# Kernel tuning notes

Hardware: AMD Instinct MI355X
Metric: run time of the kernel (lower is better)

Reference implementation:

```python
import jax, jax.numpy as jnp
import numpy as np

HID = 2048      # hidden_size
NH = 32         # num_heads
G = 8           # num_kv_groups
R = NH // G     # repeat factor (heads per kv group)
HD = HID // NH  # head_dim = 64
SCALE = HD ** 0.5


def setup_inputs() -> dict:
    key = jax.random.key(0)
    ks = jax.random.split(key, 10)
    B, S = 2, 1024
    x = jax.random.normal(ks[0], (B, S, HID), dtype=jnp.float32)
    attention_mask = jnp.ones((B, S, S), dtype=jnp.float32)
    # Linear params stored as [in, out] (y = x @ W + b), same math as torch Linear.
    Wq = jax.random.normal(ks[1], (HID, HID), dtype=jnp.float32) * 0.02
    bq = jnp.zeros((HID,), dtype=jnp.float32)
    Wk = jax.random.normal(ks[2], (HID, G * HD), dtype=jnp.float32) * 0.02
    bk = jnp.zeros((G * HD,), dtype=jnp.float32)
    Wv = jax.random.normal(ks[3], (HID, G * HD), dtype=jnp.float32) * 0.02
    bv = jnp.zeros((G * HD,), dtype=jnp.float32)
    Wo = jax.random.normal(ks[4], (HID, HID), dtype=jnp.float32) * 0.02
    bo = jnp.zeros((HID,), dtype=jnp.float32)
    return {"x": x, "attention_mask": attention_mask,
            "Wq": Wq, "bq": bq, "Wk": Wk, "bk": bk,
            "Wv": Wv, "bv": bv, "Wo": Wo, "bo": bo}


def reference(x, attention_mask, Wq, bq, Wk, bk, Wv, bv, Wo, bo):
    B, S, _ = x.shape
    # Projections. Group heads as (G, R) instead of repeat_interleave:
    # repeat_interleave(key, R, dim=2) duplicates each kv group R times, which is
    # exactly sharing key[:, :, g] across the R heads of group g.
    q = (x @ Wq + bq).reshape(B, S, G, R, HD)   # [B,S,G,R,HD] (heads = G*R in order)
    k = (x @ Wk + bk).reshape(B, S, G, HD)      # [B,S,G,HD]
    v = (x @ Wv + bv).reshape(B, S, G, HD)
    # scores [B,G,R,Sq,Sk] == torch's [B, NH, Sq, Sk] with NH = G*R
    scores = jnp.einsum('bqgrd,bkgd->bgrqk', q, k) / SCALE
    scores = scores * attention_mask[:, None, None]  # multiplicative mask per head
    w = jax.nn.softmax(scores, axis=-1)
    out = jnp.einsum('bgrqk,bkgd->bqgrd', w, v).reshape(B, S, HID)
    return out @ Wo + bo + x
```

## Files before the change

### kernel.cpp

```cpp
#include <hip/hip_runtime.h>

typedef unsigned short u16;
typedef unsigned int u32;
typedef __attribute__((ext_vector_type(8))) short bf16x8;
typedef __attribute__((ext_vector_type(4))) float f32x4;

#define HID 2048
#define S_LEN 1024
#define BATCH 2
#define G_KV 8
#define R_REP 4
#define HD 64
#define NQKV 3072

__device__ __forceinline__ u16 f2bf(float f) {
    union { u32 u; float ff; } x; x.ff = f;
    u32 u = x.u;
    u += 0x7FFFu + ((u >> 16) & 1u);
    return (u16)(u >> 16);
}
__device__ __forceinline__ float bf2f(u16 v) {
    union { u32 u; float f; } x; x.u = ((u32)v) << 16; return x.f;
}

__device__ __forceinline__ void gload_lds16(const void* g, void* l) {
    __builtin_amdgcn_global_load_lds((const __attribute__((address_space(1))) void*)g,
                                     (__attribute__((address_space(3))) void*)l,
                                     16, 0, 0);
}

__global__ __launch_bounds__(256) void cvt_x(const float* __restrict__ in,
                                             u16* __restrict__ out) {
    int i = (blockIdx.x * 256 + threadIdx.x) * 8;
    float4 a = *(const float4*)(in + i);
    float4 b = *(const float4*)(in + i + 4);
    u16 t[8] = {f2bf(a.x), f2bf(a.y), f2bf(a.z), f2bf(a.w),
                f2bf(b.x), f2bf(b.y), f2bf(b.z), f2bf(b.w)};
    *(uint4*)(out + i) = *(const uint4*)t;
}

__global__ __launch_bounds__(256) void transpose_cvt(const float* __restrict__ in,
                                                     u16* __restrict__ out,
                                                     int K, int N) {
    __shared__ float tile[32][33];
    int n0 = blockIdx.x * 32, k0 = blockIdx.y * 32;
    int tx = threadIdx.x, ty = threadIdx.y;
#pragma unroll
    for (int j = 0; j < 4; ++j)
        tile[ty + j * 8][tx] = in[(size_t)(k0 + ty + j * 8) * N + n0 + tx];
    __syncthreads();
#pragma unroll
    for (int j = 0; j < 4; ++j)
        out[(size_t)(n0 + ty + j * 8) * K + k0 + tx] = f2bf(tile[tx][ty + j * 8]);
}

__global__ __launch_bounds__(256) void gemm_qkv(const u16* __restrict__ Xb,
                                                const u16* __restrict__ WT,
                                                const float* __restrict__ bq,
                                                const float* __restrict__ bk,
                                                const float* __restrict__ bv,
                                                u16* __restrict__ qb,
                                                u16* __restrict__ kb,
                                                u16* __restrict__ vb) {
    __shared__ __align__(16) u16 As[128 * 32];
    __shared__ __align__(16) u16 Bs[128 * 32];
    int tid = threadIdx.x;
    int w = tid >> 6, lane = tid & 63, quad = lane >> 4, l16 = lane & 15;
    int m0 = blockIdx.y * 128, n0 = blockIdx.x * 128;
    int wr = (w >> 1) * 64, wc = (w & 1) * 64;
    int srow = lane >> 2, scol = (lane & 3) * 8;

    f32x4 acc[4][4];
#pragma unroll
    for (int i = 0; i < 4; ++i)
#pragma unroll
        for (int j = 0; j < 4; ++j) acc[i][j] = (f32x4){0.f, 0.f, 0.f, 0.f};

    for (int k0 = 0; k0 < 2048; k0 += 32) {
#pragma unroll
        for (int c = 0; c < 2; ++c) {
            int row = c * 64 + w * 16 + srow;
            gload_lds16(&Xb[(size_t)(m0 + row) * 2048 + k0 + scol], &As[(c * 64 + w * 16) * 32]);
            gload_lds16(&WT[(size_t)(n0 + row) * 2048 + k0 + scol], &Bs[(c * 64 + w * 16) * 32]);
        }
        __syncthreads();
        bf16x8 af[4], bfr[4];
#pragma unroll
        for (int mt = 0; mt < 4; ++mt)
            af[mt] = *(const bf16x8*)&As[(wr + mt * 16 + l16) * 32 + quad * 8];
#pragma unroll
        for (int nt = 0; nt < 4; ++nt)
            bfr[nt] = *(const bf16x8*)&Bs[(wc + nt * 16 + l16) * 32 + quad * 8];
#pragma unroll
        for (int mt = 0; mt < 4; ++mt)
#pragma unroll
            for (int nt = 0; nt < 4; ++nt)
                acc[mt][nt] = __builtin_amdgcn_mfma_f32_16x16x32_bf16(af[mt], bfr[nt], acc[mt][nt], 0, 0, 0);
        __syncthreads();
    }

#pragma unroll
    for (int nt = 0; nt < 4; ++nt) {
        int n = n0 + wc + nt * 16 + l16;
        float bias;
        if (n < 2048) bias = bq[n];
        else if (n < 2560) bias = bk[n - 2048];
        else bias = bv[n - 2560];
#pragma unroll
        for (int mt = 0; mt < 4; ++mt) {
#pragma unroll
            for (int reg = 0; reg < 4; ++reg) {
                int m = m0 + wr + mt * 16 + quad * 4 + reg;
                float val = acc[mt][nt][reg] + bias;
                int b = m >> 10, s = m & 1023;
                if (n < 2048) {
                    int g = n >> 8, r = (n >> 6) & 3, d = n & 63;
                    qb[((((size_t)(b * G_KV + g) * R_REP + r) * S_LEN) + s) * HD + d] = f2bf(val * 0.125f);
                } else if (n < 2560) {
                    int n2 = n - 2048, g = n2 >> 6, d = n2 & 63;
                    kb[(((size_t)(b * G_KV + g) * S_LEN) + s) * HD + d] = f2bf(val);
                } else {
                    int n2 = n - 2560, g = n2 >> 6, d = n2 & 63;
                    vb[(((size_t)(b * G_KV + g) * HD + d) * S_LEN) + s] = f2bf(val);
                }
            }
        }
    }
}

__global__ __launch_bounds__(256) void attn_mfma(const u16* __restrict__ qbuf,
                                                 const u16* __restrict__ kbuf,
                                                 const u16* __restrict__ vtbuf,
                                                 const u16* __restrict__ mask_bf,
                                                 u16* __restrict__ aout) {
    __shared__ __align__(16) u16 Ks[64 * 72];
    __shared__ __align__(16) u16 Vs[64 * 72];
    __shared__ __align__(16) u16 Ms[64 * 72];
    __shared__ __align__(16) u16 Ps[64 * 72];

    int d = blockIdx.x;
    int xcd = d & 7, j = d >> 3;
    int pr = xcd * 2 + (j >> 6);
    int r = (j >> 4) & 3, qblk = j & 15;
    int b = pr >> 3, g = pr & 7;

    int tid = threadIdx.x;
    int w = tid >> 6, lane = tid & 63, quad = lane >> 4, l16 = lane & 15;
    int s0 = qblk * 64;

    const u16* qrow = qbuf +
        ((((size_t)(b * G_KV + g) * R_REP + r) * S_LEN) + s0 + w * 16 + l16) * HD;
    bf16x8 qf0 = *(const bf16x8*)(qrow + quad * 8);
    bf16x8 qf1 = *(const bf16x8*)(qrow + 32 + quad * 8);

    f32x4 o_acc[4];
#pragma unroll
    for (int i = 0; i < 4; ++i) o_acc[i] = (f32x4){0.f, 0.f, 0.f, 0.f};
    float l_tot[4] = {0.f, 0.f, 0.f, 0.f};

    const u16* kbase  = kbuf  + (size_t)(b * G_KV + g) * S_LEN * HD;
    const u16* vtbase = vtbuf + (size_t)(b * G_KV + g) * HD * S_LEN;
    const u16* mbase  = mask_bf + ((size_t)b * S_LEN + s0) * S_LEN;

    int srow = tid >> 2, sc = (tid & 3) * 16;
    int prow = w * 16 + quad * 4;

    uint4 kp0, kp1, vp0, vp1, mp0, mp1;
    {
        const u16* kr = kbase + (size_t)srow * HD + sc;
        kp0 = *(const uint4*)kr; kp1 = *(const uint4*)(kr + 8);
        const u16* vr = vtbase + (size_t)srow * S_LEN + sc;
        vp0 = *(const uint4*)vr; vp1 = *(const uint4*)(vr + 8);
        const u16* mr = mbase + (size_t)srow * S_LEN + sc;
        mp0 = *(const uint4*)mr; mp1 = *(const uint4*)(mr + 8);
    }

    for (int kt = 0; kt < 16; ++kt) {
        __syncthreads();
        *(uint4*)&Ks[srow * 72 + sc]     = kp0;
        *(uint4*)&Ks[srow * 72 + sc + 8] = kp1;
        *(uint4*)&Vs[srow * 72 + sc]     = vp0;
        *(uint4*)&Vs[srow * 72 + sc + 8] = vp1;
        *(uint4*)&Ms[srow * 72 + sc]     = mp0;
        *(uint4*)&Ms[srow * 72 + sc + 8] = mp1;
        __syncthreads();

        if (kt < 15) {
            int nk = (kt + 1) * 64;
            const u16* kr = kbase + (size_t)(nk + srow) * HD + sc;
            kp0 = *(const uint4*)kr; kp1 = *(const uint4*)(kr + 8);
            const u16* vr = vtbase + (size_t)srow * S_LEN + nk + sc;
            vp0 = *(const uint4*)vr; vp1 = *(const uint4*)(vr + 8);
            const u16* mr = mbase + (size_t)srow * S_LEN + nk + sc;
            mp0 = *(const uint4*)mr; mp1 = *(const uint4*)(mr + 8);
        }

        f32x4 p[4];
#pragma unroll
        for (int nt = 0; nt < 4; ++nt) {
            bf16x8 kf0 = *(const bf16x8*)&Ks[(nt * 16 + l16) * 72 + quad * 8];
            bf16x8 kf1 = *(const bf16x8*)&Ks[(nt * 16 + l16) * 72 + 32 + quad * 8];
            f32x4 z = (f32x4){0.f, 0.f, 0.f, 0.f};
            z = __builtin_amdgcn_mfma_f32_16x16x32_bf16(qf0, kf0, z, 0, 0, 0);
            p[nt] = __builtin_amdgcn_mfma_f32_16x16x32_bf16(qf1, kf1, z, 0, 0, 0);
        }

        float part[4] = {0.f, 0.f, 0.f, 0.f};
#pragma unroll
        for (int nt = 0; nt < 4; ++nt) {
#pragma unroll
            for (int reg = 0; reg < 4; ++reg) {
                int qr = prow + reg;
                float m = bf2f(Ms[qr * 72 + nt * 16 + l16]);
                float e = __expf(p[nt][reg] * m);
                part[reg] += e;
                Ps[qr * 72 + nt * 16 + l16] = f2bf(e);
            }
        }
        __syncthreads();

#pragma unroll
        for (int reg = 0; reg < 4; ++reg) {
            float v = part[reg];
            v += __shfl_xor(v, 1);
            v += __shfl_xor(v, 2);
            v += __shfl_xor(v, 4);
            v += __shfl_xor(v, 8);
            l_tot[reg] += v;
        }

        bf16x8 pf0 = *(const bf16x8*)&Ps[(w * 16 + l16) * 72 + quad * 8];
        bf16x8 pf1 = *(const bf16x8*)&Ps[(w * 16 + l16) * 72 + 32 + quad * 8];
#pragma unroll
        for (int nt = 0; nt < 4; ++nt) {
            bf16x8 vf0 = *(const bf16x8*)&Vs[(nt * 16 + l16) * 72 + quad * 8];
            bf16x8 vf1 = *(const bf16x8*)&Vs[(nt * 16 + l16) * 72 + 32 + quad * 8];
            o_acc[nt] = __builtin_amdgcn_mfma_f32_16x16x32_bf16(pf0, vf0, o_acc[nt], 0, 0, 0);
            o_acc[nt] = __builtin_amdgcn_mfma_f32_16x16x32_bf16(pf1, vf1, o_acc[nt], 0, 0, 0);
        }
    }

#pragma unroll
    for (int reg = 0; reg < 4; ++reg) {
        int row = prow + reg;
        float inv = 1.0f / l_tot[reg];
        int sidx = s0 + row;
        u16* dst = aout + ((size_t)(b * S_LEN + sidx)) * HID + (g * R_REP + r) * HD;
#pragma unroll
        for (int nt = 0; nt < 4; ++nt)
            dst[nt * 16 + l16] = f2bf(o_acc[nt][reg] * inv);
    }
}

__global__ __launch_bounds__(256) void gemm_o(const u16* __restrict__ A,
                                              const u16* __restrict__ WT,
                                              const float* __restrict__ bo,
                                              const float* __restrict__ Xres,
                                              float* __restrict__ out) {
    __shared__ __align__(16) u16 As[128 * 32];
    __shared__ __align__(16) u16 Bs[128 * 32];
    int tid = threadIdx.x;
    int w = tid >> 6, lane = tid & 63, quad = lane >> 4, l16 = lane & 15;
    int m0 = blockIdx.y * 128, n0 = blockIdx.x * 128;
    int wr = (w >> 1) * 64, wc = (w & 1) * 64;
    int srow = lane >> 2, scol = (lane & 3) * 8;

    f32x4 acc[4][4];
#pragma unroll
    for (int i = 0; i < 4; ++i)
#pragma unroll
        for (int j = 0; j < 4; ++j) acc[i][j] = (f32x4){0.f, 0.f, 0.f, 0.f};

    for (int k0 = 0; k0 < 2048; k0 += 32) {
#pragma unroll
        for (int c = 0; c < 2; ++c) {
            int row = c * 64 + w * 16 + srow;
            gload_lds16(&A[(size_t)(m0 + row) * 2048 + k0 + scol],  &As[(c * 64 + w * 16) * 32]);
            gload_lds16(&WT[(size_t)(n0 + row) * 2048 + k0 + scol], &Bs[(c * 64 + w * 16) * 32]);
        }
        __syncthreads();
        bf16x8 af[4], bfr[4];
#pragma unroll
        for (int mt = 0; mt < 4; ++mt)
            af[mt] = *(const bf16x8*)&As[(wr + mt * 16 + l16) * 32 + quad * 8];
#pragma unroll
        for (int nt = 0; nt < 4; ++nt)
            bfr[nt] = *(const bf16x8*)&Bs[(wc + nt * 16 + l16) * 32 + quad * 8];
#pragma unroll
        for (int mt = 0; mt < 4; ++mt)
#pragma unroll
            for (int nt = 0; nt < 4; ++nt)
                acc[mt][nt] = __builtin_amdgcn_mfma_f32_16x16x32_bf16(af[mt], bfr[nt], acc[mt][nt], 0, 0, 0);
        __syncthreads();
    }

#pragma unroll
    for (int nt = 0; nt < 4; ++nt) {
        int n = n0 + wc + nt * 16 + l16;
        float bias = bo[n];
#pragma unroll
        for (int mt = 0; mt < 4; ++mt) {
#pragma unroll
            for (int reg = 0; reg < 4; ++reg) {
                int m = m0 + wr + mt * 16 + quad * 4 + reg;
                out[(size_t)m * 2048 + n] = acc[mt][nt][reg] + bias + Xres[(size_t)m * 2048 + n];
            }
        }
    }
}

extern "C" void kernel_launch(void* const* d_in, const int* in_sizes, int n_in,
                              void* d_out, int out_size, void* d_ws, size_t ws_size,
                              hipStream_t stream) {
    const float* x    = (const float*)d_in[0];
    const float* mask = (const float*)d_in[1];
    const float* Wq   = (const float*)d_in[2];
    const float* bq   = (const float*)d_in[3];
    const float* Wk   = (const float*)d_in[4];
    const float* bk   = (const float*)d_in[5];
    const float* Wv   = (const float*)d_in[6];
    const float* bv   = (const float*)d_in[7];
    const float* Wo   = (const float*)d_in[8];
    const float* bo   = (const float*)d_in[9];
    float* out = (float*)d_out;

    u16* ws = (u16*)d_ws;
    size_t off = 0;
    u16* WqkvT = ws + off; off += (size_t)NQKV * 2048;
    u16* WoT   = ws + off; off += (size_t)2048 * 2048;
    u16* q_buf = ws + off; off += (size_t)BATCH * G_KV * R_REP * S_LEN * HD;
    u16* k_buf = ws + off; off += (size_t)BATCH * G_KV * S_LEN * HD;
    u16* v_buf = ws + off; off += (size_t)BATCH * G_KV * S_LEN * HD;
    u16* a_out = ws + off; off += (size_t)2048 * 2048;
    u16* Xb      = a_out;
    u16* mask_bf = WqkvT;

    cvt_x<<<dim3(2048 * 2048 / (256 * 8)), 256, 0, stream>>>(x, Xb);

    dim3 tb(32, 8);
    transpose_cvt<<<dim3(64, 64), tb, 0, stream>>>(Wq, WqkvT, 2048, 2048);
    transpose_cvt<<<dim3(16, 64), tb, 0, stream>>>(Wk, WqkvT + (size_t)2048 * 2048, 2048, 512);
    transpose_cvt<<<dim3(16, 64), tb, 0, stream>>>(Wv, WqkvT + (size_t)2560 * 2048, 2048, 512);
    transpose_cvt<<<dim3(64, 64), tb, 0, stream>>>(Wo, WoT, 2048, 2048);

    gemm_qkv<<<dim3(NQKV / 128, 2048 / 128), 256, 0, stream>>>(Xb, WqkvT, bq, bk, bv,
                                                               q_buf, k_buf, v_buf);

    cvt_x<<<dim3(BATCH * S_LEN * S_LEN / (256 * 8)), 256, 0, stream>>>(mask, mask_bf);

    attn_mfma<<<dim3(BATCH * G_KV * R_REP * (S_LEN / 64)), 256, 0, stream>>>(
        q_buf, k_buf, v_buf, mask_bf, a_out);

    gemm_o<<<dim3(2048 / 128, 2048 / 128), 256, 0, stream>>>(a_out, WoT, bo, x, out);
}
```

Before: 273.0 us.

## Pre-permute mask into MFMA fragment order to bypass LDS staging

Replaces the flat bf16 mask conversion with a kernel that reorders each 64x64 mask tile into the per-lane MFMA accumulator layout. The attention kernel can then load each thread's 16 mask values directly from global memory into registers, dropping the Ms shared-memory buffer along with its stores and scattered reads. This cuts LDS traffic and shared-memory footprint in the attention loop. The cost is a more complex preprocessing kernel that stages tiles through shared memory.

After: 265.0 us. 1.03x faster.

```diff
diff --git a/kernel.cpp b/kernel.cpp
--- a/kernel.cpp
+++ b/kernel.cpp
@@ -37,6 +37,31 @@
     u16 t[8] = {f2bf(a.x), f2bf(a.y), f2bf(a.z), f2bf(a.w),
                 f2bf(b.x), f2bf(b.y), f2bf(b.z), f2bf(b.w)};
     *(uint4*)(out + i) = *(const uint4*)t;
+}
+
+__global__ __launch_bounds__(256) void mask_perm(const float* __restrict__ mask,
+                                                 u16* __restrict__ out) {
+    __shared__ float tile[64 * 68];
+    int bid = blockIdx.x;
+    int kt = bid & 15, qblk = (bid >> 4) & 15, b = bid >> 8;
+    int t = threadIdx.x;
+    int row = t >> 2, c0 = (t & 3) * 16;
+    const float* src = mask + ((size_t)b * S_LEN + qblk * 64 + row) * S_LEN + kt * 64 + c0;
+#pragma unroll
+    for (int i = 0; i < 4; ++i)
+        *(float4*)&tile[row * 68 + c0 + i * 4] = *(const float4*)(src + i * 4);
+    __syncthreads();
+    int w = t >> 6, quad = (t >> 4) & 3, l16 = t & 15;
+    int prow = w * 16 + quad * 4;
+    u16 v[16];
+#pragma unroll
+    for (int nt = 0; nt < 4; ++nt)
+#pragma unroll
+        for (int reg = 0; reg < 4; ++reg)
+            v[nt * 4 + reg] = f2bf(tile[(prow + reg) * 68 + nt * 16 + l16]);
+    u16* dst = out + ((size_t)bid) * 4096 + t * 16;
+    *(uint4*)dst = ((uint4*)v)[0];
+    *(uint4*)(dst + 8) = ((uint4*)v)[1];
 }
 
 __global__ __launch_bounds__(256) void transpose_cvt(const float* __restrict__ in,
@@ -131,11 +156,10 @@
 __global__ __launch_bounds__(256) void attn_mfma(const u16* __restrict__ qbuf,
                                                  const u16* __restrict__ kbuf,
                                                  const u16* __restrict__ vtbuf,
-                                                 const u16* __restrict__ mask_bf,
+                                                 const u16* __restrict__ mask_pm,
                                                  u16* __restrict__ aout) {
     __shared__ __align__(16) u16 Ks[64 * 72];
     __shared__ __align__(16) u16 Vs[64 * 72];
-    __shared__ __align__(16) u16 Ms[64 * 72];
     __shared__ __align__(16) u16 Ps[64 * 72];
 
     int d = blockIdx.x;
@@ -160,7 +184,7 @@
 
     const u16* kbase  = kbuf  + (size_t)(b * G_KV + g) * S_LEN * HD;
     const u16* vtbase = vtbuf + (size_t)(b * G_KV + g) * HD * S_LEN;
-    const u16* mbase  = mask_bf + ((size_t)b * S_LEN + s0) * S_LEN;
+    const u16* mbase  = mask_pm + ((size_t)(b * 16 + qblk) * 16) * 4096 + tid * 16;
 
     int srow = tid >> 2, sc = (tid & 3) * 16;
     int prow = w * 16 + quad * 4;
@@ -171,8 +195,7 @@
         kp0 = *(const uint4*)kr; kp1 = *(const uint4*)(kr + 8);
         const u16* vr = vtbase + (size_t)srow * S_LEN + sc;
         vp0 = *(const uint4*)vr; vp1 = *(const uint4*)(vr + 8);
-        const u16* mr = mbase + (size_t)srow * S_LEN + sc;
-        mp0 = *(const uint4*)mr; mp1 = *(const uint4*)(mr + 8);
+        mp0 = *(const uint4*)mbase; mp1 = *(const uint4*)(mbase + 8);
     }
 
     for (int kt = 0; kt < 16; ++kt) {
@@ -181,8 +204,7 @@
         *(uint4*)&Ks[srow * 72 + sc + 8] = kp1;
         *(uint4*)&Vs[srow * 72 + sc]     = vp0;
         *(uint4*)&Vs[srow * 72 + sc + 8] = vp1;
-        *(uint4*)&Ms[srow * 72 + sc]     = mp0;
-        *(uint4*)&Ms[srow * 72 + sc + 8] = mp1;
+        uint4 m0c = mp0, m1c = mp1;
         __syncthreads();
 
         if (kt < 15) {
@@ -191,7 +213,7 @@
             kp0 = *(const uint4*)kr; kp1 = *(const uint4*)(kr + 8);
             const u16* vr = vtbase + (size_t)srow * S_LEN + nk + sc;
             vp0 = *(const uint4*)vr; vp1 = *(const uint4*)(vr + 8);
-            const u16* mr = mbase + (size_t)srow * S_LEN + nk + sc;
+            const u16* mr = mbase + (size_t)(kt + 1) * 4096;
             mp0 = *(const uint4*)mr; mp1 = *(const uint4*)(mr + 8);
         }
 
@@ -205,16 +227,18 @@
             p[nt] = __builtin_amdgcn_mfma_f32_16x16x32_bf16(qf1, kf1, z, 0, 0, 0);
         }
 
+        const u16* mv0 = (const u16*)&m0c;
+        const u16* mv1 = (const u16*)&m1c;
         float part[4] = {0.f, 0.f, 0.f, 0.f};
 #pragma unroll
         for (int nt = 0; nt < 4; ++nt) {
 #pragma unroll
             for (int reg = 0; reg < 4; ++reg) {
-                int qr = prow + reg;
-                float m = bf2f(Ms[qr * 72 + nt * 16 + l16]);
+                int idx = nt * 4 + reg;
+                float m = bf2f(idx < 8 ? mv0[idx] : mv1[idx - 8]);
                 float e = __expf(p[nt][reg] * m);
                 part[reg] += e;
-                Ps[qr * 72 + nt * 16 + l16] = f2bf(e);
+                Ps[(prow + reg) * 72 + nt * 16 + l16] = f2bf(e);
             }
         }
         __syncthreads();
@@ -333,7 +357,7 @@
     u16* v_buf = ws + off; off += (size_t)BATCH * G_KV * S_LEN * HD;
     u16* a_out = ws + off; off += (size_t)2048 * 2048;
     u16* Xb      = a_out;
-    u16* mask_bf = WqkvT;
+    u16* mask_pm = WqkvT;
 
     cvt_x<<<dim3(2048 * 2048 / (256 * 8)), 256, 0, stream>>>(x, Xb);
 
@@ -346,10 +370,10 @@
     gemm_qkv<<<dim3(NQKV / 128, 2048 / 128), 256, 0, stream>>>(Xb, WqkvT, bq, bk, bv,
                                                                q_buf, k_buf, v_buf);
 
-    cvt_x<<<dim3(BATCH * S_LEN * S_LEN / (256 * 8)), 256, 0, stream>>>(mask, mask_bf);
+    mask_perm<<<dim3(BATCH * 16 * 16), 256, 0, stream>>>(mask, mask_pm);
 
     attn_mfma<<<dim3(BATCH * G_KV * R_REP * (S_LEN / 64)), 256, 0, stream>>>(
-        q_buf, k_buf, v_buf, mask_bf, a_out);
+        q_buf, k_buf, v_buf, mask_pm, a_out);
 
     gemm_o<<<dim3(2048 / 128, 2048 / 128), 256, 0, stream>>>(a_out, WoT, bo, x, out);
 }
```
